# Kernel optimization log

Measured on AMD Instinct MI355X. Metric: run time of the kernel, lower is better.

The kernel has to match this reference:

```python
import jax, jax.numpy as jnp
import numpy as np

B, S, D = 4, 512, 4096
H, G = 32, 8           # num_heads, num_groups (GQA)
HD = D // H            # head_dim = 128
REP = H // G           # query heads per kv group = 4


def rotate_half(x):
    x1, x2 = x[..., : x.shape[-1] // 2], x[..., x.shape[-1] // 2 :]
    return jnp.concatenate([-x2, x1], axis=-1)


def setup_inputs() -> dict:
    key = jax.random.key(0)
    ks = jax.random.split(key, 5)
    return {
        "x": jax.random.normal(ks[0], (B, S, D), dtype=jnp.float32),
        "wq": jax.random.normal(ks[1], (D, D), dtype=jnp.float32) * 0.02,
        "bq": jnp.zeros((D,), dtype=jnp.float32),
        "wk": jax.random.normal(ks[2], (D, G * HD), dtype=jnp.float32) * 0.02,
        "bk": jnp.zeros((G * HD,), dtype=jnp.float32),
        "wv": jax.random.normal(ks[3], (D, G * HD), dtype=jnp.float32) * 0.02,
        "bv": jnp.zeros((G * HD,), dtype=jnp.float32),
        "wo": jax.random.normal(ks[4], (D, D), dtype=jnp.float32) * 0.02,
        "bo": jnp.zeros((D,), dtype=jnp.float32),
    }


def reference(x, wq, bq, wk, bk, wv, bv, wo, bo):
    b, s, d = x.shape
    q = (x @ wq + bq).reshape(b, s, H, HD)
    k = (x @ wk + bk).reshape(b, s, G, HD)
    v = (x @ wv + bv).reshape(b, s, G, HD)

    # RoPE tables (identical to module's cached sin/cos, sliced to seq len)
    inv_freq = 1.0 / (10000.0 ** (jnp.arange(0, HD, 2, dtype=jnp.float32) / HD))
    freqs = jnp.outer(jnp.arange(s, dtype=jnp.float32), inv_freq)  # [s, HD/2]
    freqs = jnp.concatenate([freqs, freqs], axis=-1)               # [s, HD]
    sin = jnp.sin(freqs)[:, None, :]  # [s, 1, HD] broadcast over heads
    cos = jnp.cos(freqs)[:, None, :]

    q = q * cos + rotate_half(q) * sin
    k = k * cos + rotate_half(k) * sin

    # Module scales q by HD**-0.5 AND jax.nn.dot_product_attention applies its
    # own default 1/sqrt(HD) -> net logit scale is HD**-1. Reproduce exactly.
    scale = HD ** (-0.5)
    q = q * scale

    # GQA without materializing repeated k/v: group query heads.
    qg = q.reshape(b, s, G, REP, HD)
    logits = jnp.einsum("bqgrd,bkgd->bgrqk", qg, k) * scale  # second scale (SDPA default)
    attn = jax.nn.softmax(logits, axis=-1)
    out = jnp.einsum("bgrqk,bkgd->bqgrd", attn, v).reshape(b, s, d)
    return out @ wo + bo
```

## Files before the change

kernel.cpp:

```cpp
#include <hip/hip_runtime.h>
#include <math.h>

typedef unsigned short ushort_t;
typedef __attribute__((ext_vector_type(8))) short bf16x8;
typedef __attribute__((ext_vector_type(4))) float f32x4;
typedef __attribute__((ext_vector_type(4))) unsigned short us4;
typedef __attribute__((ext_vector_type(8))) unsigned short us8;

#define B_   4
#define S_   512
#define D_   4096
#define H_   32
#define G_   8
#define HD_  128
#define KV_  1024
#define M_   (B_ * S_)
#define QN_  6144

__device__ __forceinline__ float bf2f(ushort_t u) {
    union { unsigned u; float f; } x; x.u = ((unsigned)u) << 16; return x.f;
}
__device__ __forceinline__ ushort_t f2bf(float f) {
    union { float f; unsigned u; } x; x.f = f;
    unsigned r = x.u + 0x7fffu + ((x.u >> 16) & 1u);
    return (ushort_t)(r >> 16);
}

typedef const __attribute__((address_space(1))) void* gptr_t;
typedef __attribute__((address_space(3))) void* ldsptr_t;

__device__ __forceinline__ void gload_lds16(const void* g, void* lds) {
    __builtin_amdgcn_global_load_lds((gptr_t)g, (ldsptr_t)lds, 16, 0, 0);
}

#define BAR() asm volatile("s_barrier" ::: "memory")

__global__ void xconv(const float* __restrict__ x, ushort_t* __restrict__ xb, int n8)
{
    const int i = blockIdx.x * blockDim.x + threadIdx.x;
    if (i >= n8) return;
    const float4 a = *(const float4*)&x[(size_t)i * 8];
    const float4 b = *(const float4*)&x[(size_t)i * 8 + 4];
    us8 o;
    o[0] = f2bf(a.x); o[1] = f2bf(a.y); o[2] = f2bf(a.z); o[3] = f2bf(a.w);
    o[4] = f2bf(b.x); o[5] = f2bf(b.y); o[6] = f2bf(b.z); o[7] = f2bf(b.w);
    *(us8*)&xb[(size_t)i * 8] = o;
}

__global__ __launch_bounds__(256) void wconv_all(
    const float* __restrict__ wq, const float* __restrict__ wk,
    const float* __restrict__ wv, ushort_t* __restrict__ Wt)
{
    __shared__ float t[32][33];
    const int n0 = blockIdx.x * 32, k0 = blockIdx.y * 32;
    const float* W; int nsrc, N;
    if (n0 < 4096)      { W = wq; nsrc = n0;        N = 4096; }
    else if (n0 < 5120) { W = wk; nsrc = n0 - 4096; N = 1024; }
    else                { W = wv; nsrc = n0 - 5120; N = 1024; }
    const int tid = threadIdx.x;
    const int r = tid >> 3, c4 = (tid & 7) * 4;
    const float4 v = *(const float4*)&W[(size_t)(k0 + r) * N + nsrc + c4];
    t[r][c4 + 0] = v.x; t[r][c4 + 1] = v.y; t[r][c4 + 2] = v.z; t[r][c4 + 3] = v.w;
    __syncthreads();
    us4 o;
    o.x = f2bf(t[c4 + 0][r]);
    o.y = f2bf(t[c4 + 1][r]);
    o.z = f2bf(t[c4 + 2][r]);
    o.w = f2bf(t[c4 + 3][r]);
    *(us4*)&Wt[(size_t)(n0 + r) * D_ + k0 + c4] = o;
}

__global__ __launch_bounds__(256) void wconv(
    const float* __restrict__ W, ushort_t* __restrict__ Wt, int K, int N)
{
    __shared__ float t[32][33];
    const int n0 = blockIdx.x * 32, k0 = blockIdx.y * 32;
    const int tid = threadIdx.x;
    const int r = tid >> 3, c4 = (tid & 7) * 4;
    const float4 v = *(const float4*)&W[(size_t)(k0 + r) * N + n0 + c4];
    t[r][c4 + 0] = v.x; t[r][c4 + 1] = v.y; t[r][c4 + 2] = v.z; t[r][c4 + 3] = v.w;
    __syncthreads();
    us4 o;
    o.x = f2bf(t[c4 + 0][r]);
    o.y = f2bf(t[c4 + 1][r]);
    o.z = f2bf(t[c4 + 2][r]);
    o.w = f2bf(t[c4 + 3][r]);
    *(us4*)&Wt[(size_t)(n0 + r) * K + k0 + c4] = o;
}

template<int OUT_BF16, int SPLITK, int ROPE>
__global__ __launch_bounds__(512, 2) void gemm8(
    const ushort_t* __restrict__ A, int lda,
    const ushort_t* __restrict__ Bt, int ldb,
    const float* __restrict__ bias0, const float* __restrict__ bias1,
    const float* __restrict__ bias2,
    float* __restrict__ Cf, ushort_t* __restrict__ Cb,
    float* __restrict__ P0, float* __restrict__ P1,
    int M, int N, int K)
{
    __shared__ ushort_t sA[2][256 * 64];
    __shared__ ushort_t sB[2][256 * 64];

    const int tid = threadIdx.x;
    const int lane = tid & 63, w = tid >> 6;
    const int lr = lane & 15, kg = lane >> 4;
    const int wr = w >> 2, wc = w & 3;

    const int nwg = gridDim.x;
    const int cpx = nwg >> 3;
    const int bid = (blockIdx.x & 7) * cpx + (blockIdx.x >> 3);
    int khalf = 0, tile = bid;
    if (SPLITK) { khalf = bid >> 7; tile = bid & 127; }
    const int nbx = N >> 8;
    const int bx = tile % nbx, by = tile / nbx;
    const int bm0 = by << 8, bn0 = bx << 8;
    if (SPLITK) { A += (size_t)khalf * K; Bt += (size_t)khalf * K; }

    const int NT = K >> 6;

    const ushort_t* gp[4][2];
    char*           lp[4][2];
    #pragma unroll
    for (int h = 0; h < 4; ++h) {
        const ushort_t* gb; int ld; char* sbase;
        if (h < 2) { gb = A + (size_t)bm0 * lda; ld = lda; sbase = (char*)sA; }
        else       { gb = Bt + (size_t)bn0 * ldb; ld = ldb; sbase = (char*)sB; }
        const int half = h & 1;
        #pragma unroll
        for (int j = 0; j < 2; ++j) {
            const int o = j * 8192 + tid * 16;
            const int row = half * 128 + (o >> 7);
            const int slot = (o >> 4) & 7;
            gp[h][j] = gb + (size_t)row * ld + ((slot ^ (row & 7)) << 3);
            lp[h][j] = sbase + half * 16384 + j * 8192 + w * 1024;
        }
    }
    auto stage = [&](int t, int h, int c) {
        #pragma unroll
        for (int j = 0; j < 2; ++j)
            gload_lds16(gp[h][j] + t * 64, lp[h][j] + c * 32768);
    };
    auto lda_frag = [&](int c, int mi, int s) {
        const int row = mi * 32 + wr * 16 + lr;
        return *(const bf16x8*)((const char*)sA + c * 32768 + row * 128 +
                                (((s * 4 + kg) ^ (row & 7)) << 4));
    };
    auto ldb_frag = [&](int c, int ni, int s) {
        const int row = ni * 64 + wc * 16 + lr;
        return *(const bf16x8*)((const char*)sB + c * 32768 + row * 128 +
                                (((s * 4 + kg) ^ (row & 7)) << 4));
    };

    f32x4 acc[8][4];
    #pragma unroll
    for (int i = 0; i < 8; ++i)
        #pragma unroll
        for (int j = 0; j < 4; ++j)
            acc[i][j] = (f32x4){0.f, 0.f, 0.f, 0.f};

    stage(0, 0, 0); stage(0, 2, 0); stage(0, 3, 0); stage(0, 1, 0);
    stage(1, 0, 1); stage(1, 2, 1); stage(1, 3, 1);
    asm volatile("s_waitcnt vmcnt(6)" ::: "memory");
    BAR();

    auto iter = [&](int t, int c) {
        bf16x8 a[4][2], b[4][2];

        #pragma unroll
        for (int ni = 0; ni < 2; ++ni)
            #pragma unroll
            for (int s = 0; s < 2; ++s) b[ni][s] = ldb_frag(c, ni, s);
        #pragma unroll
        for (int mi = 0; mi < 4; ++mi)
            #pragma unroll
            for (int s = 0; s < 2; ++s) a[mi][s] = lda_frag(c, mi, s);
        if (t + 1 < NT) stage(t + 1, 1, c ^ 1);
        BAR();
        __builtin_amdgcn_s_setprio(1);
        #pragma unroll
        for (int mi = 0; mi < 4; ++mi)
            #pragma unroll
            for (int ni = 0; ni < 2; ++ni)
                #pragma unroll
                for (int s = 0; s < 2; ++s)
                    acc[mi][ni] = __builtin_amdgcn_mfma_f32_16x16x32_bf16(
                        a[mi][s], b[ni][s], acc[mi][ni], 0, 0, 0);
        __builtin_amdgcn_s_setprio(0);
        BAR();

        #pragma unroll
        for (int ni = 2; ni < 4; ++ni)
            #pragma unroll
            for (int s = 0; s < 2; ++s) b[ni][s] = ldb_frag(c, ni, s);
        if (t + 2 < NT) stage(t + 2, 0, c);
        BAR();
        __builtin_amdgcn_s_setprio(1);
        #pragma unroll
        for (int mi = 0; mi < 4; ++mi)
            #pragma unroll
            for (int ni = 2; ni < 4; ++ni)
                #pragma unroll
                for (int s = 0; s < 2; ++s)
                    acc[mi][ni] = __builtin_amdgcn_mfma_f32_16x16x32_bf16(
                        a[mi][s], b[ni][s], acc[mi][ni], 0, 0, 0);
        __builtin_amdgcn_s_setprio(0);
        BAR();

        #pragma unroll
        for (int mi = 0; mi < 4; ++mi)
            #pragma unroll
            for (int s = 0; s < 2; ++s) a[mi][s] = lda_frag(c, mi + 4, s);
        if (t + 2 < NT) stage(t + 2, 2, c);
        BAR();
        __builtin_amdgcn_s_setprio(1);
        #pragma unroll
        for (int mi = 0; mi < 4; ++mi)
            #pragma unroll
            for (int ni = 2; ni < 4; ++ni)
                #pragma unroll
                for (int s = 0; s < 2; ++s)
                    acc[mi + 4][ni] = __builtin_amdgcn_mfma_f32_16x16x32_bf16(
                        a[mi][s], b[ni][s], acc[mi + 4][ni], 0, 0, 0);
        __builtin_amdgcn_s_setprio(0);
        BAR();

        if (t + 2 < NT) {
            stage(t + 2, 3, c);
            asm volatile("s_waitcnt vmcnt(6)" ::: "memory");
        } else {
            asm volatile("s_waitcnt vmcnt(0)" ::: "memory");
        }
        BAR();
        __builtin_amdgcn_s_setprio(1);
        #pragma unroll
        for (int mi = 0; mi < 4; ++mi)
            #pragma unroll
            for (int ni = 0; ni < 2; ++ni)
                #pragma unroll
                for (int s = 0; s < 2; ++s)
                    acc[mi + 4][ni] = __builtin_amdgcn_mfma_f32_16x16x32_bf16(
                        a[mi][s], b[ni][s], acc[mi + 4][ni], 0, 0, 0);
        __builtin_amdgcn_s_setprio(0);
        BAR();
    };

    for (int t = 0; t < NT; t += 2) { iter(t, 0); iter(t + 1, 1); }

    if (ROPE && bn0 < 5120) {
        const float scale = (bn0 < 4096) ? (1.f / 128.f) : 1.f;
        const int jj = wc * 16 + lr;
        const float invf = __expf(-0.1439115683121279f * (float)jj);
        #pragma unroll
        for (int mi = 0; mi < 8; ++mi) {
            const int mr = bm0 + mi * 32 + wr * 16 + kg * 4;
            #pragma unroll
            for (int r = 0; r < 4; ++r) {
                const int srow = (mr + r) & 511;
                float sn, cs;
                __sincosf((float)srow * invf, &sn, &cs);
                #pragma unroll
                for (int nip = 0; nip < 2; ++nip) {
                    const int n_lo = bn0 + nip * 128 + jj;
                    const int n_hi = n_lo + 64;
                    const float b_lo = (n_lo < 4096) ? bias0[n_lo]
                                     : (n_lo < 5120) ? bias1[n_lo - 4096] : bias2[n_lo - 5120];
                    const float b_hi = (n_hi < 4096) ? bias0[n_hi]
                                     : (n_hi < 5120) ? bias1[n_hi - 4096] : bias2[n_hi - 5120];
                    const float a_lo = acc[mi][nip * 2][r] + b_lo;
                    const float a_hi = acc[mi][nip * 2 + 1][r] + b_hi;
                    Cb[(size_t)(mr + r) * N + n_lo] = f2bf((a_lo * cs - a_hi * sn) * scale);
                    Cb[(size_t)(mr + r) * N + n_hi] = f2bf((a_hi * cs + a_lo * sn) * scale);
                }
            }
        }
        return;
    }
    #pragma unroll
    for (int mi = 0; mi < 8; ++mi) {
        #pragma unroll
        for (int ni = 0; ni < 4; ++ni) {
            const int n = bn0 + ni * 64 + wc * 16 + lr;
            const float bs = (n < 4096) ? bias0[n]
                           : (n < 5120) ? bias1[n - 4096] : bias2[n - 5120];
            const int mr = bm0 + mi * 32 + wr * 16 + kg * 4;
            #pragma unroll
            for (int r = 0; r < 4; ++r) {
                if (SPLITK) {
                    const int row = mr + r;
                    if (khalf == 0) {
                        Cf[(size_t)row * N + n] = acc[mi][ni][r] + bs;
                    } else {
                        float* P = (row < 1024) ? P0 : P1;
                        P[((size_t)(row & 1023) << 12) + n] = acc[mi][ni][r];
                    }
                } else {
                    const float val = acc[mi][ni][r] + bs;
                    if (OUT_BF16) Cb[(size_t)(mr + r) * N + n] = f2bf(val);
                    else          Cf[(size_t)(mr + r) * N + n] = val;
                }
            }
        }
    }
}

__global__ void reduce_add(const float* __restrict__ P0, const float* __restrict__ P1,
                           float* __restrict__ out)
{
    const int n4 = M_ * D_ / 4;
    for (int i4 = blockIdx.x * blockDim.x + threadIdx.x; i4 < n4;
         i4 += gridDim.x * blockDim.x) {
        const float4 p = (i4 < (1 << 20))
            ? *(const float4*)&P0[(size_t)i4 * 4]
            : *(const float4*)&P1[(size_t)(i4 - (1 << 20)) * 4];
        float4 o = *(float4*)&out[(size_t)i4 * 4];
        o.x += p.x; o.y += p.y; o.z += p.z; o.w += p.w;
        *(float4*)&out[(size_t)i4 * 4] = o;
    }
}

__global__ __launch_bounds__(256) void vtrans(
    const ushort_t* __restrict__ vb,
    ushort_t* __restrict__ vT)
{
    __shared__ ushort_t t[32][40];
    const int s0 = blockIdx.x * 32;
    const int d0 = blockIdx.y * 32;
    const int bg = blockIdx.z;
    const int b = bg >> 3, g = bg & 7;
    const int tid = threadIdx.x;
    const int row = tid >> 3, c4 = (tid & 7) * 4;
    const us4 v = *(const us4*)&vb[(size_t)(b * S_ + s0 + row) * QN_ + g * HD_ + d0 + c4];
    t[row][c4 + 0] = v.x; t[row][c4 + 1] = v.y;
    t[row][c4 + 2] = v.z; t[row][c4 + 3] = v.w;
    __syncthreads();
    us4 o;
    o.x = t[c4 + 0][row]; o.y = t[c4 + 1][row];
    o.z = t[c4 + 2][row]; o.w = t[c4 + 3][row];
    *(us4*)&vT[(size_t)(bg * HD_ + d0 + row) * S_ + s0 + c4] = o;
}

__global__ __launch_bounds__(256) void attn_mfma(
    const ushort_t* __restrict__ kb,
    const ushort_t* __restrict__ vT,
    ushort_t* __restrict__ qb)
{
    __shared__ ushort_t sKV[8192];
    __shared__ ushort_t sP[4 * 16 * 512];

    const int q0 = blockIdx.x * 64;
    const int h = blockIdx.y, b = blockIdx.z;
    const int g = h >> 2;
    const int tid = threadIdx.x;
    const int lane = tid & 63, w = tid >> 6;
    const int lr = lane & 15, kg = lane >> 4;

    bf16x8 af[4];
    {
        const ushort_t* qrow = qb + (size_t)(b * S_ + q0 + w * 16 + lr) * QN_ + h * HD_;
        #pragma unroll
        for (int c = 0; c < 4; ++c)
            af[c] = *(const bf16x8*)(qrow + c * 32 + kg * 8);
    }

    f32x4 l[8][4];
    #pragma unroll
    for (int ch = 0; ch < 8; ++ch)
        #pragma unroll
        for (int t = 0; t < 4; ++t)
            l[ch][t] = (f32x4){0.f, 0.f, 0.f, 0.f};

    const ushort_t* kbase = kb + (size_t)b * S_ * QN_ + g * HD_;
    #pragma unroll
    for (int ch = 0; ch < 8; ++ch) {
        __syncthreads();
        #pragma unroll
        for (int i = 0; i < 4; ++i) {
            const int o = w * 4096 + i * 1024;
            const int key = (o >> 8) + (lane >> 4);
            const int sl = lane & 15;
            gload_lds16(kbase + (size_t)(ch * 64 + key) * QN_ + ((sl ^ (key & 15)) * 8),
                        (char*)sKV + o);
        }
        __syncthreads();
        #pragma unroll
        for (int t = 0; t < 4; ++t) {
            const int key = t * 16 + lr;
            #pragma unroll
            for (int c = 0; c < 4; ++c) {
                const bf16x8 bf = *(const bf16x8*)((const char*)sKV + key * 256 +
                                                   (((c * 4 + kg) ^ (key & 15)) << 4));
                l[ch][t] = __builtin_amdgcn_mfma_f32_16x16x32_bf16(af[c], bf, l[ch][t], 0, 0, 0);
            }
        }
    }

    float inv[4];
    #pragma unroll
    for (int r = 0; r < 4; ++r) {
        float m = -1e30f;
        #pragma unroll
        for (int ch = 0; ch < 8; ++ch)
            #pragma unroll
            for (int t = 0; t < 4; ++t)
                m = fmaxf(m, l[ch][t][r]);
        #pragma unroll
        for (int msk = 1; msk <= 8; msk <<= 1)
            m = fmaxf(m, __shfl_xor(m, msk));
        float s = 0.f;
        const int q = kg * 4 + r;
        #pragma unroll
        for (int ch = 0; ch < 8; ++ch)
            #pragma unroll
            for (int t = 0; t < 4; ++t) {
                const float p = __expf(l[ch][t][r] - m);
                s += p;
                const int gs = ch * 8 + t * 2 + (lr >> 3);
                sP[w * 8192 + q * 512 + ((gs ^ q) << 3) + (lr & 7)] = f2bf(p);
            }
        #pragma unroll
        for (int msk = 1; msk <= 8; msk <<= 1)
            s += __shfl_xor(s, msk);
        inv[r] = 1.f / s;
    }

    f32x4 oacc[8];
    #pragma unroll
    for (int dt = 0; dt < 8; ++dt) oacc[dt] = (f32x4){0.f, 0.f, 0.f, 0.f};

    const ushort_t* vbase = vT + (size_t)(b * G_ + g) * HD_ * S_;
    for (int ch = 0; ch < 8; ++ch) {
        __syncthreads();
        #pragma unroll
        for (int i = 0; i < 4; ++i) {
            const int o = w * 4096 + i * 1024;
            const int d = (o >> 7) + (lane >> 3);
            const int sl = lane & 7;
            gload_lds16(vbase + (size_t)d * S_ + ch * 64 + ((sl ^ (d & 7)) * 8),
                        (char*)sKV + o);
        }
        __syncthreads();
        #pragma unroll
        for (int c2 = 0; c2 < 2; ++c2) {
            const int gs = ch * 8 + c2 * 4 + kg;
            const bf16x8 ap = *(const bf16x8*)((const char*)sP + w * 16384 + lr * 1024 +
                                               ((gs ^ lr) << 4));
            #pragma unroll
            for (int dt = 0; dt < 8; ++dt) {
                const int d = dt * 16 + lr;
                const bf16x8 bv = *(const bf16x8*)((const char*)sKV + d * 128 +
                                                   (((c2 * 4 + kg) ^ (d & 7)) << 4));
                oacc[dt] = __builtin_amdgcn_mfma_f32_16x16x32_bf16(ap, bv, oacc[dt], 0, 0, 0);
            }
        }
    }

    #pragma unroll
    for (int dt = 0; dt < 8; ++dt) {
        #pragma unroll
        for (int r = 0; r < 4; ++r) {
            const int q = kg * 4 + r;
            qb[(size_t)(b * S_ + q0 + w * 16 + q) * QN_ + h * HD_ + dt * 16 + lr] =
                f2bf(oacc[dt][r] * inv[r]);
        }
    }
}

extern "C" void kernel_launch(void* const* d_in, const int* in_sizes, int n_in,
                              void* d_out, int out_size, void* d_ws, size_t ws_size,
                              hipStream_t stream)
{
    const float* x  = (const float*)d_in[0];
    const float* wq = (const float*)d_in[1];
    const float* bq = (const float*)d_in[2];
    const float* wk = (const float*)d_in[3];
    const float* bk = (const float*)d_in[4];
    const float* wv = (const float*)d_in[5];
    const float* bv = (const float*)d_in[6];
    const float* wo = (const float*)d_in[7];
    const float* bo = (const float*)d_in[8];
    float* out = (float*)d_out;

    char* ws = (char*)d_ws;
    ushort_t* xb   = (ushort_t*)(ws);
    ushort_t* Wt   = (ushort_t*)(ws + (16u << 20));
    ushort_t* vT   = (ushort_t*)(ws + (48u << 20));
    ushort_t* qkv  = (ushort_t*)(ws + (64u << 20));
    float* p0      = (float*)xb;
    float* p1      = (float*)(ws + (48u << 20));

    wconv_all<<<dim3(QN_ / 32, D_ / 32), 256, 0, stream>>>(wq, wk, wv, Wt);
    xconv<<<(M_ * D_ / 8 + 255) / 256, 256, 0, stream>>>(x, xb, M_ * D_ / 8);

    gemm8<1, 0, 1><<<(QN_ / 256) * (M_ / 256), 512, 0, stream>>>(
        xb, D_, Wt, D_, bq, bk, bv, nullptr, qkv, nullptr, nullptr, M_, QN_, D_);

    vtrans<<<dim3(S_ / 32, HD_ / 32, B_ * G_), 256, 0, stream>>>(qkv + 5120, vT);

    attn_mfma<<<dim3(S_ / 64, H_, B_), 256, 0, stream>>>(qkv + 4096, vT, qkv);

    wconv<<<dim3(D_ / 32, D_ / 32), 256, 0, stream>>>(wo, Wt, D_, D_);

    gemm8<0, 1, 0><<<256, 512, 0, stream>>>(
        qkv, QN_, Wt, D_, bo, bo, bo, out, nullptr, p0, p1, M_, D_, 2048);
    reduce_add<<<2048, 256, 0, stream>>>(p0, p1, out);
}
```

Before: 312.6 us.

## Software-pipeline LDS fragment loads across GEMM phases with double-buffered B fragments

Restructures the GEMM main loop so that A-low and B-low fragments for the next K tile are loaded from LDS during the last MFMA phase of the current tile, using a double-buffered B register set. The phase order is also changed so each phase reuses fragments already in registers. The goal is to overlap LDS reads with MFMA work and remove the LDS-read stall at the start of each tile. In exchange, more fragments stay live in registers, which raises VGPR pressure and could reduce occupancy or cause spills.

Result: slower. 444.5 us (+42.2%).

```diff
diff --git a/kernel.cpp b/kernel.cpp
--- a/kernel.cpp
+++ b/kernel.cpp
@@ -151,6 +151,8 @@
                                 (((s * 4 + kg) ^ (row & 7)) << 4));
     };
 
+    bf16x8 aLo[4][2], aHi[4][2], bHi2[2][2], bLoDB[2][2][2];
+
     f32x4 acc[8][4];
     #pragma unroll
     for (int i = 0; i < 8; ++i)
@@ -162,18 +164,20 @@
     stage(1, 0, 1); stage(1, 2, 1); stage(1, 3, 1);
     asm volatile("s_waitcnt vmcnt(6)" ::: "memory");
     BAR();
+    #pragma unroll
+    for (int mi = 0; mi < 4; ++mi)
+        #pragma unroll
+        for (int s = 0; s < 2; ++s) aLo[mi][s] = lda_frag(0, mi, s);
+    #pragma unroll
+    for (int ni = 0; ni < 2; ++ni)
+        #pragma unroll
+        for (int s = 0; s < 2; ++s) bLoDB[0][ni][s] = ldb_frag(0, ni, s);
 
     auto iter = [&](int t, int c) {
-        bf16x8 a[4][2], b[4][2];
-
         #pragma unroll
         for (int ni = 0; ni < 2; ++ni)
             #pragma unroll
-            for (int s = 0; s < 2; ++s) b[ni][s] = ldb_frag(c, ni, s);
-        #pragma unroll
-        for (int mi = 0; mi < 4; ++mi)
-            #pragma unroll
-            for (int s = 0; s < 2; ++s) a[mi][s] = lda_frag(c, mi, s);
+            for (int s = 0; s < 2; ++s) bHi2[ni][s] = ldb_frag(c, ni + 2, s);
         if (t + 1 < NT) stage(t + 1, 1, c ^ 1);
         BAR();
         __builtin_amdgcn_s_setprio(1);
@@ -184,43 +188,39 @@
                 #pragma unroll
                 for (int s = 0; s < 2; ++s)
                     acc[mi][ni] = __builtin_amdgcn_mfma_f32_16x16x32_bf16(
-                        a[mi][s], b[ni][s], acc[mi][ni], 0, 0, 0);
+                        aLo[mi][s], bLoDB[c][ni][s], acc[mi][ni], 0, 0, 0);
         __builtin_amdgcn_s_setprio(0);
         BAR();
 
         #pragma unroll
-        for (int ni = 2; ni < 4; ++ni)
-            #pragma unroll
-            for (int s = 0; s < 2; ++s) b[ni][s] = ldb_frag(c, ni, s);
+        for (int mi = 0; mi < 4; ++mi)
+            #pragma unroll
+            for (int s = 0; s < 2; ++s) aHi[mi][s] = lda_frag(c, mi + 4, s);
         if (t + 2 < NT) stage(t + 2, 0, c);
         BAR();
         __builtin_amdgcn_s_setprio(1);
         #pragma unroll
         for (int mi = 0; mi < 4; ++mi)
             #pragma unroll
-            for (int ni = 2; ni < 4; ++ni)
+            for (int ni = 0; ni < 2; ++ni)
                 #pragma unroll
                 for (int s = 0; s < 2; ++s)
-                    acc[mi][ni] = __builtin_amdgcn_mfma_f32_16x16x32_bf16(
-                        a[mi][s], b[ni][s], acc[mi][ni], 0, 0, 0);
+                    acc[mi][ni + 2] = __builtin_amdgcn_mfma_f32_16x16x32_bf16(
+                        aLo[mi][s], bHi2[ni][s], acc[mi][ni + 2], 0, 0, 0);
         __builtin_amdgcn_s_setprio(0);
         BAR();
 
+        if (t + 2 < NT) stage(t + 2, 2, c);
+        BAR();
+        __builtin_amdgcn_s_setprio(1);
         #pragma unroll
         for (int mi = 0; mi < 4; ++mi)
             #pragma unroll
-            for (int s = 0; s < 2; ++s) a[mi][s] = lda_frag(c, mi + 4, s);
-        if (t + 2 < NT) stage(t + 2, 2, c);
-        BAR();
-        __builtin_amdgcn_s_setprio(1);
-        #pragma unroll
-        for (int mi = 0; mi < 4; ++mi)
-            #pragma unroll
-            for (int ni = 2; ni < 4; ++ni)
+            for (int ni = 0; ni < 2; ++ni)
                 #pragma unroll
                 for (int s = 0; s < 2; ++s)
-                    acc[mi + 4][ni] = __builtin_amdgcn_mfma_f32_16x16x32_bf16(
-                        a[mi][s], b[ni][s], acc[mi + 4][ni], 0, 0, 0);
+                    acc[mi + 4][ni + 2] = __builtin_amdgcn_mfma_f32_16x16x32_bf16(
+                        aHi[mi][s], bHi2[ni][s], acc[mi + 4][ni + 2], 0, 0, 0);
         __builtin_amdgcn_s_setprio(0);
         BAR();
 
@@ -231,6 +231,14 @@
             asm volatile("s_waitcnt vmcnt(0)" ::: "memory");
         }
         BAR();
+        #pragma unroll
+        for (int mi = 0; mi < 4; ++mi)
+            #pragma unroll
+            for (int s = 0; s < 2; ++s) aLo[mi][s] = lda_frag(c ^ 1, mi, s);
+        #pragma unroll
+        for (int ni = 0; ni < 2; ++ni)
+            #pragma unroll
+            for (int s = 0; s < 2; ++s) bLoDB[c ^ 1][ni][s] = ldb_frag(c ^ 1, ni, s);
         __builtin_amdgcn_s_setprio(1);
         #pragma unroll
         for (int mi = 0; mi < 4; ++mi)
@@ -239,7 +247,7 @@
                 #pragma unroll
                 for (int s = 0; s < 2; ++s)
                     acc[mi + 4][ni] = __builtin_amdgcn_mfma_f32_16x16x32_bf16(
-                        a[mi][s], b[ni][s], acc[mi + 4][ni], 0, 0, 0);
+                        aHi[mi][s], bLoDB[c][ni][s], acc[mi + 4][ni], 0, 0, 0);
         __builtin_amdgcn_s_setprio(0);
         BAR();
     };
```

## Add dedicated 128x384-tile QKV GEMM with fused RoPE epilogue

Applied to the files above, without the earlier changes.

Replaces the generic 256x256-tile gemm8 for the QKV projection with a specialised kernel using 128x384 tiles, giving exactly 256 blocks (M=2048/128 × N=6144/384) to match the CU count. It also swizzles the block-to-tile mapping across XCDs and pipelines B-tile loads in three chunks interleaved with MFMA phases. The intent is to remove the partial wave of the previous 192-block grid and improve load balance. The trade-off is lower arithmetic intensity per tile and a more complex RoPE/bias epilogue with per-segment branching.

Result: no change. 310.8 us (median of 3 runs) (-0.6%).

```diff
diff --git a/kernel.cpp b/kernel.cpp
--- a/kernel.cpp
+++ b/kernel.cpp
@@ -88,6 +88,177 @@
     *(us4*)&Wt[(size_t)(n0 + r) * K + k0 + c4] = o;
 }
 
+__global__ __launch_bounds__(512, 2) void gemm_qkv(
+    const ushort_t* __restrict__ A,
+    const ushort_t* __restrict__ Bt,
+    const float* __restrict__ bias0, const float* __restrict__ bias1,
+    const float* __restrict__ bias2,
+    ushort_t* __restrict__ Cb)
+{
+    __shared__ ushort_t sA[2][128 * 64];
+    __shared__ ushort_t sB[2][384 * 64];
+
+    const int tid = threadIdx.x;
+    const int lane = tid & 63, w = tid >> 6;
+    const int lr = lane & 15, kg = lane >> 4;
+    const int wr = w >> 2, wc = w & 3;
+
+    const int bid = (blockIdx.x & 7) * 32 + (blockIdx.x >> 3);
+    const int bx = bid & 15, by = bid >> 4;
+    const int bm0 = by << 7, bn0 = bx * 384;
+
+    const int NT = 64;
+    const int lda = D_, ldb = D_, N = QN_;
+
+    const ushort_t* gp[4][2];
+    char*           lp[4][2];
+    #pragma unroll
+    for (int u = 0; u < 4; ++u) {
+        #pragma unroll
+        for (int j = 0; j < 2; ++j) {
+            const int o = j * 8192 + tid * 16;
+            const int row = o >> 7, slot = (o >> 4) & 7;
+            if (u == 0) {
+                gp[u][j] = A + (size_t)(bm0 + row) * lda + ((slot ^ (row & 7)) << 3);
+                lp[u][j] = (char*)sA + j * 8192 + w * 1024;
+            } else {
+                const int brow = (u - 1) * 128 + row;
+                gp[u][j] = Bt + (size_t)(bn0 + brow) * ldb + ((slot ^ (row & 7)) << 3);
+                lp[u][j] = (char*)sB + (u - 1) * 16384 + j * 8192 + w * 1024;
+            }
+        }
+    }
+    auto stage = [&](int t, int u, int c) {
+        const int coff = (u == 0) ? c * 16384 : c * 49152;
+        #pragma unroll
+        for (int j = 0; j < 2; ++j)
+            gload_lds16(gp[u][j] + t * 64, lp[u][j] + coff);
+    };
+    auto lda_frag = [&](int c, int mi, int s) {
+        const int row = mi * 32 + wr * 16 + lr;
+        return *(const bf16x8*)((const char*)sA + c * 16384 + row * 128 +
+                                (((s * 4 + kg) ^ (row & 7)) << 4));
+    };
+    auto ldb_frag = [&](int c, int ni, int s) {
+        const int row = ni * 64 + wc * 16 + lr;
+        return *(const bf16x8*)((const char*)sB + c * 49152 + row * 128 +
+                                (((s * 4 + kg) ^ (row & 7)) << 4));
+    };
+
+    f32x4 acc[4][6];
+    #pragma unroll
+    for (int i = 0; i < 4; ++i)
+        #pragma unroll
+        for (int j = 0; j < 6; ++j)
+            acc[i][j] = (f32x4){0.f, 0.f, 0.f, 0.f};
+
+    stage(0, 0, 0); stage(0, 1, 0); stage(0, 2, 0); stage(0, 3, 0);
+    stage(1, 0, 1); stage(1, 1, 1); stage(1, 2, 1);
+    asm volatile("s_waitcnt vmcnt(6)" ::: "memory");
+    BAR();
+
+    auto iter = [&](int t, int c) {
+        bf16x8 a[4][2], b[2][2];
+
+        #pragma unroll
+        for (int ni = 0; ni < 2; ++ni)
+            #pragma unroll
+            for (int s = 0; s < 2; ++s) b[ni][s] = ldb_frag(c, ni, s);
+        #pragma unroll
+        for (int mi = 0; mi < 4; ++mi)
+            #pragma unroll
+            for (int s = 0; s < 2; ++s) a[mi][s] = lda_frag(c, mi, s);
+        if (t + 1 < NT) stage(t + 1, 3, c ^ 1);
+        BAR();
+        __builtin_amdgcn_s_setprio(1);
+        #pragma unroll
+        for (int mi = 0; mi < 4; ++mi)
+            #pragma unroll
+            for (int ni = 0; ni < 2; ++ni)
+                #pragma unroll
+                for (int s = 0; s < 2; ++s)
+                    acc[mi][ni] = __builtin_amdgcn_mfma_f32_16x16x32_bf16(
+                        a[mi][s], b[ni][s], acc[mi][ni], 0, 0, 0);
+        __builtin_amdgcn_s_setprio(0);
+        BAR();
+
+        #pragma unroll
+        for (int ni = 0; ni < 2; ++ni)
+            #pragma unroll
+            for (int s = 0; s < 2; ++s) b[ni][s] = ldb_frag(c, ni + 2, s);
+        if (t + 2 < NT) { stage(t + 2, 0, c); stage(t + 2, 1, c); }
+        BAR();
+        __builtin_amdgcn_s_setprio(1);
+        #pragma unroll
+        for (int mi = 0; mi < 4; ++mi)
+            #pragma unroll
+            for (int ni = 0; ni < 2; ++ni)
+                #pragma unroll
+                for (int s = 0; s < 2; ++s)
+                    acc[mi][ni + 2] = __builtin_amdgcn_mfma_f32_16x16x32_bf16(
+                        a[mi][s], b[ni][s], acc[mi][ni + 2], 0, 0, 0);
+        __builtin_amdgcn_s_setprio(0);
+        BAR();
+
+        #pragma unroll
+        for (int ni = 0; ni < 2; ++ni)
+            #pragma unroll
+            for (int s = 0; s < 2; ++s) b[ni][s] = ldb_frag(c, ni + 4, s);
+        if (t + 2 < NT) {
+            stage(t + 2, 2, c);
+            asm volatile("s_waitcnt vmcnt(6)" ::: "memory");
+        } else {
+            asm volatile("s_waitcnt vmcnt(0)" ::: "memory");
+        }
+        BAR();
+        __builtin_amdgcn_s_setprio(1);
+        #pragma unroll
+        for (int mi = 0; mi < 4; ++mi)
+            #pragma unroll
+            for (int ni = 0; ni < 2; ++ni)
+                #pragma unroll
+                for (int s = 0; s < 2; ++s)
+                    acc[mi][ni + 4] = __builtin_amdgcn_mfma_f32_16x16x32_bf16(
+                        a[mi][s], b[ni][s], acc[mi][ni + 4], 0, 0, 0);
+        __builtin_amdgcn_s_setprio(0);
+        BAR();
+    };
+
+    for (int t = 0; t < NT; t += 2) { iter(t, 0); iter(t + 1, 1); }
+
+    const int jj = wc * 16 + lr;
+    const float invf = __expf(-0.1439115683121279f * (float)jj);
+    #pragma unroll
+    for (int mi = 0; mi < 4; ++mi) {
+        const int mr = bm0 + mi * 32 + wr * 16 + kg * 4;
+        #pragma unroll
+        for (int r = 0; r < 4; ++r) {
+            const int srow = (mr + r) & 511;
+            float sn, cs;
+            __sincosf((float)srow * invf, &sn, &cs);
+            #pragma unroll
+            for (int nip = 0; nip < 3; ++nip) {
+                const int pb = bn0 + nip * 128;
+                const int n_lo = pb + jj, n_hi = n_lo + 64;
+                const float b_lo = (n_lo < 4096) ? bias0[n_lo]
+                                 : (n_lo < 5120) ? bias1[n_lo - 4096] : bias2[n_lo - 5120];
+                const float b_hi = (n_hi < 4096) ? bias0[n_hi]
+                                 : (n_hi < 5120) ? bias1[n_hi - 4096] : bias2[n_hi - 5120];
+                const float a_lo = acc[mi][nip * 2][r] + b_lo;
+                const float a_hi = acc[mi][nip * 2 + 1][r] + b_hi;
+                if (pb < 5120) {
+                    const float scale = (pb < 4096) ? (1.f / 128.f) : 1.f;
+                    Cb[(size_t)(mr + r) * N + n_lo] = f2bf((a_lo * cs - a_hi * sn) * scale);
+                    Cb[(size_t)(mr + r) * N + n_hi] = f2bf((a_hi * cs + a_lo * sn) * scale);
+                } else {
+                    Cb[(size_t)(mr + r) * N + n_lo] = f2bf(a_lo);
+                    Cb[(size_t)(mr + r) * N + n_hi] = f2bf(a_hi);
+                }
+            }
+        }
+    }
+}
+
 template<int OUT_BF16, int SPLITK, int ROPE>
 __global__ __launch_bounds__(512, 2) void gemm8(
     const ushort_t* __restrict__ A, int lda,
@@ -246,35 +417,6 @@
 
     for (int t = 0; t < NT; t += 2) { iter(t, 0); iter(t + 1, 1); }
 
-    if (ROPE && bn0 < 5120) {
-        const float scale = (bn0 < 4096) ? (1.f / 128.f) : 1.f;
-        const int jj = wc * 16 + lr;
-        const float invf = __expf(-0.1439115683121279f * (float)jj);
-        #pragma unroll
-        for (int mi = 0; mi < 8; ++mi) {
-            const int mr = bm0 + mi * 32 + wr * 16 + kg * 4;
-            #pragma unroll
-            for (int r = 0; r < 4; ++r) {
-                const int srow = (mr + r) & 511;
-                float sn, cs;
-                __sincosf((float)srow * invf, &sn, &cs);
-                #pragma unroll
-                for (int nip = 0; nip < 2; ++nip) {
-                    const int n_lo = bn0 + nip * 128 + jj;
-                    const int n_hi = n_lo + 64;
-                    const float b_lo = (n_lo < 4096) ? bias0[n_lo]
-                                     : (n_lo < 5120) ? bias1[n_lo - 4096] : bias2[n_lo - 5120];
-                    const float b_hi = (n_hi < 4096) ? bias0[n_hi]
-                                     : (n_hi < 5120) ? bias1[n_hi - 4096] : bias2[n_hi - 5120];
-                    const float a_lo = acc[mi][nip * 2][r] + b_lo;
-                    const float a_hi = acc[mi][nip * 2 + 1][r] + b_hi;
-                    Cb[(size_t)(mr + r) * N + n_lo] = f2bf((a_lo * cs - a_hi * sn) * scale);
-                    Cb[(size_t)(mr + r) * N + n_hi] = f2bf((a_hi * cs + a_lo * sn) * scale);
-                }
-            }
-        }
-        return;
-    }
     #pragma unroll
     for (int mi = 0; mi < 8; ++mi) {
         #pragma unroll
@@ -491,8 +633,7 @@
     wconv_all<<<dim3(QN_ / 32, D_ / 32), 256, 0, stream>>>(wq, wk, wv, Wt);
     xconv<<<(M_ * D_ / 8 + 255) / 256, 256, 0, stream>>>(x, xb, M_ * D_ / 8);
 
-    gemm8<1, 0, 1><<<(QN_ / 256) * (M_ / 256), 512, 0, stream>>>(
-        xb, D_, Wt, D_, bq, bk, bv, nullptr, qkv, nullptr, nullptr, M_, QN_, D_);
+    gemm_qkv<<<256, 512, 0, stream>>>(xb, Wt, bq, bk, bv, qkv);
 
     vtrans<<<dim3(S_ / 32, HD_ / 32, B_ * G_), 256, 0, stream>>>(qkv + 5120, vT);
 
```
